# Kernel optimization log

Measured on AMD Instinct MI355X. Metric: run time of the kernel, lower is better.

The kernel has to match this reference:

```python
import jax, jax.numpy as jnp
import numpy as np

NLAT, NLON = 64, 64
CIN = 512
HEADS = 8


def _cc_weights(n):
    # Clenshaw-Curtis quadrature weights on [-1, 1] for nodes cos(k*pi/(n-1)),
    # as used by torch-harmonics for the 'equiangular' grid. Weights sum to 2.
    N = n - 1
    theta = np.pi * np.arange(n) / N
    m = N // 2
    j = np.arange(1, m + 1)
    b = np.where(2 * j == N, 1.0, 2.0)
    S = (b / (4.0 * j ** 2 - 1.0))[None, :] * np.cos(2.0 * j[None, :] * theta[:, None])
    w = 1.0 - S.sum(axis=1)
    c = np.full(n, 2.0)
    c[0] = 1.0
    c[-1] = 1.0
    return c * w / N


def _log_quad_weights(nlat, nlon):
    # _precompute_latitudes flips nodes/weights; then 2*pi*w/nlon tiled over lon.
    w = _cc_weights(nlat)[::-1].copy()
    qw = 2.0 * np.pi * w / nlon                       # (nlat,)
    qw = np.tile(qw[:, None], (1, nlon)).reshape(-1)  # (nlat*nlon,)
    return jnp.asarray(np.log(qw), dtype=jnp.float32)


def setup_inputs() -> dict:
    key = jax.random.key(0)
    ks = jax.random.split(key, 5)
    s_qkv = float(np.sqrt(3.0 / CIN))   # scale for q/k/v 1x1-conv weights
    s_proj = float(np.sqrt(3.0 / CIN))  # out_channels == CIN
    u = lambda k, sh, s: jax.random.uniform(k, sh, jnp.float32, -s, s)
    return dict(
        query=jax.random.normal(ks[0], (1, CIN, NLAT, NLON), jnp.float32),
        q_w=u(ks[1], (CIN, CIN), s_qkv), q_b=jnp.zeros((CIN,), jnp.float32),
        k_w=u(ks[2], (CIN, CIN), s_qkv), k_b=jnp.zeros((CIN,), jnp.float32),
        v_w=u(ks[3], (CIN, CIN), s_qkv), v_b=jnp.zeros((CIN,), jnp.float32),
        p_w=u(ks[4], (CIN, CIN), s_proj), p_b=jnp.zeros((CIN,), jnp.float32),
        log_quad_weights=_log_quad_weights(NLAT, NLON),
    )


def reference(query, q_w, q_b, k_w, k_b, v_w, v_b, p_w, p_b, log_quad_weights):
    B, C, H, W = query.shape
    hd = C // HEADS  # head dim (k_channels == out_channels == in_channels)

    def proj_tokens(x, w, b):
        # 1x1 conv == channel matmul, then split heads and flatten H*W tokens
        y = jnp.einsum('bihw,oi->bohw', x, w) + b[None, :, None, None]
        return y.reshape(B, HEADS, -1, H, W).transpose(0, 1, 3, 4, 2).reshape(B, HEADS, H * W, -1)

    q = proj_tokens(query, q_w, q_b)  # (B, heads, HW, hd)
    k = proj_tokens(query, k_w, k_b)  # self-attention: key/value default to query
    v = proj_tokens(query, v_w, v_b)

    scale = 1.0 / jnp.sqrt(jnp.asarray(hd, dtype=q.dtype))
    # additive log-quadrature bias over keys (broadcast over batch/head/query)
    logits = jnp.einsum('bhqd,bhkd->bhqk', q, k) * scale + log_quad_weights[None, None, None, :]
    attn = jax.nn.softmax(logits, axis=-1)
    out = jnp.einsum('bhqk,bhkd->bhqd', attn, v)          # (B, heads, HW, hd)
    out = out.transpose(0, 1, 3, 2).reshape(B, HEADS * hd, H, W)
    return jnp.einsum('bihw,oi->bohw', out, p_w) + p_b[None, :, None, None]
```

## Files before the change

kernel.cpp:

```cpp
#include <hip/hip_runtime.h>

typedef unsigned short u16;
typedef unsigned int u32;
typedef __bf16 bf16x8 __attribute__((ext_vector_type(8)));
typedef float f32x4 __attribute__((ext_vector_type(4)));
typedef unsigned short u16x4 __attribute__((ext_vector_type(4)));

#define LOG2E 1.4426950408889634f

#if __has_builtin(__builtin_amdgcn_exp2f)
#define EXP2F(x) __builtin_amdgcn_exp2f(x)
#else
#define EXP2F(x) exp2f(x)
#endif

__device__ __forceinline__ u16 f2bf(float f) {
    union { float f; u32 u; } a; a.f = f;
    u32 u = a.u;
    u += 0x7FFFu + ((u >> 16) & 1u);
    return (u16)(u >> 16);
}
__device__ __forceinline__ bf16x8 ldg8(const u16* p) {
    return *reinterpret_cast<const bf16x8*>(p);
}
#if __has_builtin(__builtin_amdgcn_cvt_pk_bf16_f32)
__device__ __forceinline__ u32 pack2(float a, float b) {
    auto r = __builtin_amdgcn_cvt_pk_bf16_f32(a, b);
    return __builtin_bit_cast(u32, r);
}
#else
__device__ __forceinline__ u32 pack2(float a, float b) {
    u32 ua = __float_as_uint(a) + 0x8000u;
    u32 ub = __float_as_uint(b) + 0x8000u;
    return __builtin_amdgcn_perm(ub, ua, 0x07060302);
}
#endif
__device__ __forceinline__ void async16(const void* g, void* l) {
    __builtin_amdgcn_global_load_lds(
        (const __attribute__((address_space(1))) u32*)g,
        (__attribute__((address_space(3))) u32*)l, 16, 0, 0);
}

#define MFMA16(a, b, c) __builtin_amdgcn_mfma_f32_16x16x32_bf16((a), (b), (c), 0, 0, 0)

__global__ __launch_bounds__(256) void prep(const float* __restrict__ X,
                                            u16* __restrict__ Xt,
                                            const float* __restrict__ s0,
                                            const float* __restrict__ s1,
                                            const float* __restrict__ s2,
                                            const float* __restrict__ s3,
                                            u16* __restrict__ Wqkv,
                                            u16* __restrict__ Wp,
                                            const float* __restrict__ lqw,
                                            float* __restrict__ lqw2g) {
    __shared__ u16 tile[64][65];
    const int tid = threadIdx.x;
    const int y = blockIdx.y;

    if (y < 8) {
        const int t0 = blockIdx.x * 64;
        const int c0 = y * 64;
#pragma unroll
        for (int i = 0; i < 16; ++i) {
            int idx = tid + i * 256;
            int r = idx >> 6, cc = idx & 63;
            tile[r][cc] = f2bf(X[(size_t)(c0 + r) * 4096 + t0 + cc]);
        }
        __syncthreads();
#pragma unroll
        for (int i = 0; i < 16; ++i) {
            int idx = tid + i * 256;
            int tr = idx >> 6, cc = idx & 63;
            Xt[(size_t)(t0 + tr) * 512 + c0 + cc] = tile[cc][tr];
        }
    } else if (y < 12) {
        const int m = y - 8;
        const float* s = (m == 0) ? s0 : (m == 1) ? s1 : (m == 2) ? s2 : s3;
        u16* d = (m == 3) ? Wp : Wqkv + (size_t)m * 262144;
#pragma unroll
        for (int j = 0; j < 4; ++j) {
            int i = blockIdx.x * 1024 + j * 256 + tid;
            float4 v = reinterpret_cast<const float4*>(s)[i];
            u16x4 o;
            o[0] = f2bf(v.x); o[1] = f2bf(v.y); o[2] = f2bf(v.z); o[3] = f2bf(v.w);
            reinterpret_cast<u16x4*>(d)[i] = o;
        }
    } else {
        if (blockIdx.x < 4) {
            int i = blockIdx.x * 256 + tid;
            float4 v = reinterpret_cast<const float4*>(lqw)[i];
            v.x *= LOG2E; v.y *= LOG2E; v.z *= LOG2E; v.w *= LOG2E;
            reinterpret_cast<float4*>(lqw2g)[i] = v;
        }
    }
}

__global__ __launch_bounds__(512, 2) void qkv_gemm(const u16* __restrict__ Wqkv,
                                                   const u16* __restrict__ Xt,
                                                   const float* __restrict__ qb,
                                                   const float* __restrict__ kb,
                                                   const float* __restrict__ vb,
                                                   u16* __restrict__ Qt,
                                                   u16* __restrict__ Kt,
                                                   u16* __restrict__ Vp) {
    __shared__ __align__(16) u16 Al[2][128 * 32];
    __shared__ __align__(16) u16 Bl[2][128 * 32];

    const int tid = threadIdx.x;
    const int w = tid >> 6, lane = tid & 63;
    const int quad = lane >> 4, lm = lane & 15;
    const int wm = w & 1, wn = w >> 1;
    const int n0 = blockIdx.x * 128;
    const int my = blockIdx.y;
    const int m0 = my * 128;

    const int arow = lane >> 2;
    const int sch = (lane & 3) ^ ((lane >> 3) & 3);
    const u16* agp = Wqkv + (size_t)(m0 + w * 16 + arow) * 512 + sch * 8;
    const u16* bgp = Xt + (size_t)(n0 + w * 16 + arow) * 512 + sch * 8;

    async16(agp, &Al[0][w * 16 * 32]);
    async16(bgp, &Bl[0][w * 16 * 32]);
    agp += 32; bgp += 32;

    const int FOFF = lm * 64 + ((quad ^ ((lm >> 1) & 3)) << 4);

    f32x4 acc[4][2];
#pragma unroll
    for (int mt = 0; mt < 4; ++mt)
#pragma unroll
        for (int bt = 0; bt < 2; ++bt) acc[mt][bt] = (f32x4){0.f, 0.f, 0.f, 0.f};

    __syncthreads();

    for (int s = 0; s < 16; ++s) {
        const int buf = s & 1;
        if (s < 15) {
            async16(agp, &Al[buf ^ 1][w * 16 * 32]);
            async16(bgp, &Bl[buf ^ 1][w * 16 * 32]);
            agp += 32; bgp += 32;
        }
        const char* Ab = (const char*)&Al[buf][0];
        const char* Bb = (const char*)&Bl[buf][0];
        bf16x8 af[4], bfr[2];
#pragma unroll
        for (int mt = 0; mt < 4; ++mt)
            af[mt] = *(const bf16x8*)(Ab + wm * 4096 + mt * 1024 + FOFF);
#pragma unroll
        for (int bt = 0; bt < 2; ++bt)
            bfr[bt] = *(const bf16x8*)(Bb + wn * 2048 + bt * 1024 + FOFF);
#pragma unroll
        for (int mt = 0; mt < 4; ++mt)
#pragma unroll
            for (int bt = 0; bt < 2; ++bt)
                acc[mt][bt] = MFMA16(af[mt], bfr[bt], acc[mt][bt]);
        __syncthreads();
    }

    const int mat = my >> 2;
    const float* bias = (mat == 0) ? qb : (mat == 1) ? kb : vb;
    const int chbase = (my & 3) * 128 + wm * 64 + quad * 4;

    if (mat < 2) {
        u16* out = mat ? Kt : Qt;
        const float sc = mat ? 1.0f : 0.125f * LOG2E;
#pragma unroll
        for (int mt = 0; mt < 4; ++mt) {
            const int ch = chbase + mt * 16;
            float4 bv = *(const float4*)(bias + ch);
            float bvf[4] = {bv.x, bv.y, bv.z, bv.w};
#pragma unroll
            for (int bt = 0; bt < 2; ++bt) {
                int tok = n0 + wn * 32 + bt * 16 + lm;
                u16x4 pk;
#pragma unroll
                for (int r = 0; r < 4; ++r)
                    pk[r] = f2bf((acc[mt][bt][r] + bvf[r]) * sc);
                *(u16x4*)(out + (size_t)tok * 512 + ch) = pk;
            }
        }
    } else {
#pragma unroll
        for (int mt = 0; mt < 4; ++mt) {
            const int ch = chbase + mt * 16;
            float4 bv = *(const float4*)(bias + ch);
            float bvf[4] = {bv.x, bv.y, bv.z, bv.w};
#pragma unroll
            for (int bt = 0; bt < 2; ++bt) {
                int g = bt * 16 + lm;
                int col = n0 + wn * 32 + 8 * ((g >> 2) & 3) + 4 * ((g >> 4) & 1) + (g & 3);
#pragma unroll
                for (int r = 0; r < 4; ++r)
                    Vp[(size_t)(ch + r) * 4096 + col] = f2bf(acc[mt][bt][r] + bvf[r]);
            }
        }
    }
}

__global__ __launch_bounds__(256, 2) void out_gemm(const u16* __restrict__ Wp,
                                                   const u16* __restrict__ Ot,
                                                   const float* __restrict__ pb,
                                                   float* __restrict__ out) {
    __shared__ __align__(16) u16 Al[2][128 * 32];
    __shared__ __align__(16) u16 Bl[2][64 * 32];

    const int tid = threadIdx.x;
    const int w = tid >> 6, lane = tid & 63;
    const int quad = lane >> 4, lm = lane & 15;
    const int wm = w & 1, wn = w >> 1;
    const int n0 = blockIdx.x * 64;
    const int m0 = blockIdx.y * 128;

    const int arow = lane >> 2;
    const int sch = (lane & 3) ^ ((lane >> 3) & 3);
    const u16* agp0 = Wp + (size_t)(m0 + w * 16 + arow) * 512 + sch * 8;
    const u16* agp1 = agp0 + (size_t)64 * 512;
    const u16* bgp = Ot + (size_t)(n0 + w * 16 + arow) * 512 + sch * 8;

    async16(agp0, &Al[0][w * 16 * 32]);
    async16(agp1, &Al[0][(64 + w * 16) * 32]);
    async16(bgp, &Bl[0][w * 16 * 32]);
    agp0 += 32; agp1 += 32; bgp += 32;

    const int FOFF = lm * 64 + ((quad ^ ((lm >> 1) & 3)) << 4);

    f32x4 acc[4][2];
#pragma unroll
    for (int mt = 0; mt < 4; ++mt)
#pragma unroll
        for (int bt = 0; bt < 2; ++bt) acc[mt][bt] = (f32x4){0.f, 0.f, 0.f, 0.f};

    __syncthreads();

    for (int s = 0; s < 16; ++s) {
        const int buf = s & 1;
        if (s < 15) {
            async16(agp0, &Al[buf ^ 1][w * 16 * 32]);
            async16(agp1, &Al[buf ^ 1][(64 + w * 16) * 32]);
            async16(bgp, &Bl[buf ^ 1][w * 16 * 32]);
            agp0 += 32; agp1 += 32; bgp += 32;
        }
        const char* Ab = (const char*)&Al[buf][0];
        const char* Bb = (const char*)&Bl[buf][0];
        bf16x8 af[4], bfr[2];
#pragma unroll
        for (int mt = 0; mt < 4; ++mt)
            af[mt] = *(const bf16x8*)(Ab + wm * 4096 + mt * 1024 + FOFF);
#pragma unroll
        for (int bt = 0; bt < 2; ++bt)
            bfr[bt] = *(const bf16x8*)(Bb + wn * 2048 + bt * 1024 + FOFF);
#pragma unroll
        for (int mt = 0; mt < 4; ++mt)
#pragma unroll
            for (int bt = 0; bt < 2; ++bt)
                acc[mt][bt] = MFMA16(af[mt], bfr[bt], acc[mt][bt]);
        __syncthreads();
    }

#pragma unroll
    for (int mt = 0; mt < 4; ++mt) {
        const int ch = m0 + wm * 64 + mt * 16 + quad * 4;
        float4 bv = *(const float4*)(pb + ch);
        float bvf[4] = {bv.x, bv.y, bv.z, bv.w};
#pragma unroll
        for (int bt = 0; bt < 2; ++bt) {
            int tok = n0 + wn * 32 + bt * 16 + lm;
#pragma unroll
            for (int r = 0; r < 4; ++r)
                out[(size_t)(ch + r) * 4096 + tok] = acc[mt][bt][r] + bvf[r];
        }
    }
}

__global__ __launch_bounds__(512, 4) void flash_attn(const u16* __restrict__ Qt,
                                                     const u16* __restrict__ Kt,
                                                     const u16* __restrict__ Vp,
                                                     const float* __restrict__ lqw2g,
                                                     u16* __restrict__ Ot) {
    __shared__ __align__(16) u16 kv[4][2][2][2048];

    const int tid = threadIdx.x;
    const int w = tid >> 6, lane = tid & 63;
    const int quad = lane >> 4, lm = lane & 15;
    const int qg = w & 1, quarter = w >> 1;
    const int h = blockIdx.y, hq = h * 64;
    const int q0 = blockIdx.x * 64 + qg * 32;
    const int kstart = quarter * 1024;

    char* kvb = (char*)&kv[0][0][0][0] + quarter * 16384;

    const int srow = lane >> 3;
    const int schunk = (lane & 7) ^ srow;
    const u16* kgp = Kt + (size_t)(kstart + qg * 16 + srow) * 512 + hq + schunk * 8;
    const u16* kgp8 = kgp + (size_t)8 * 512;
    const int dloc0 = qg * 32 + 2 * srow + (schunk >> 2);
    const u16* vgpA = Vp + (size_t)(hq + dloc0) * 4096 + kstart + (schunk & 3) * 8;
    const u16* vgpB = vgpA + (size_t)16 * 4096;

    {
        char* nb = kvb;
        async16(kgp, nb + qg * 2048);
        async16(kgp8, nb + qg * 2048 + 1024);
        async16(vgpA, nb + 4096 + qg * 2048);
        async16(vgpB, nb + 4096 + qg * 2048 + 1024);
        kgp += 32 * 512; kgp8 += 32 * 512; vgpA += 32; vgpB += 32;
    }

    const int A0 = lm * 128 + ((quad ^ (lm & 7)) << 4);
    const int A1 = A0 ^ 64;
    const int AV = (lm >> 1) * 128 +
                   ((((4 * (lm & 1) + quad)) ^ ((lm >> 1) & 7)) << 4);

    const u16* qbase = Qt + (size_t)(q0 + lm) * 512 + hq + quad * 8;
    const bf16x8 bq0a = ldg8(qbase);
    const bf16x8 bq1a = ldg8(qbase + 32);
    const bf16x8 bq0b = ldg8(qbase + 16 * 512);
    const bf16x8 bq1b = ldg8(qbase + 16 * 512 + 32);

    union { u32 u[4]; bf16x8 v; } onesu;
    onesu.u[0] = onesu.u[1] = onesu.u[2] = onesu.u[3] = 0x3F803F80u;
    const bf16x8 onesv = onesu.v;

    f32x4 acc_o[4][2];
#pragma unroll
    for (int mt = 0; mt < 4; ++mt) {
        acc_o[mt][0] = (f32x4){0.f, 0.f, 0.f, 0.f};
        acc_o[mt][1] = (f32x4){0.f, 0.f, 0.f, 0.f};
    }
    f32x4 acc_l[2];
    acc_l[0] = (f32x4){0.f, 0.f, 0.f, 0.f};
    acc_l[1] = (f32x4){0.f, 0.f, 0.f, 0.f};

    __syncthreads();

#define ATTN_STEP(BUF, KT0, DO_STAGE)                                          \
    {                                                                          \
        if (DO_STAGE) {                                                        \
            char* nb = kvb + (((BUF) ^ 1) * 8192);                             \
            async16(kgp, nb + qg * 2048);                                      \
            async16(kgp8, nb + qg * 2048 + 1024);                              \
            async16(vgpA, nb + 4096 + qg * 2048);                              \
            async16(vgpB, nb + 4096 + qg * 2048 + 1024);                       \
            kgp += 32 * 512; kgp8 += 32 * 512; vgpA += 32; vgpB += 32;         \
        }                                                                      \
        const char* Kb = kvb + (BUF) * 8192;                                   \
        const char* Vb = Kb + 4096;                                            \
        u32 pk[2][2][2];                                                       \
        _Pragma("unroll")                                                      \
        for (int nt = 0; nt < 2; ++nt) {                                       \
            bf16x8 k0 = *(const bf16x8*)(Kb + nt * 2048 + A0);                 \
            bf16x8 k1 = *(const bf16x8*)(Kb + nt * 2048 + A1);                 \
            f32x4 bias = *(const f32x4*)(lqw2g + (KT0) + nt * 16 + quad * 4);  \
            f32x4 a0 = MFMA16(k0, bq0a, bias);                                 \
            a0 = MFMA16(k1, bq1a, a0);                                         \
            f32x4 a1 = MFMA16(k0, bq0b, bias);                                 \
            a1 = MFMA16(k1, bq1b, a1);                                         \
            pk[nt][0][0] = pack2(EXP2F(a0[0]), EXP2F(a0[1]));                  \
            pk[nt][0][1] = pack2(EXP2F(a0[2]), EXP2F(a0[3]));                  \
            pk[nt][1][0] = pack2(EXP2F(a1[0]), EXP2F(a1[1]));                  \
            pk[nt][1][1] = pack2(EXP2F(a1[2]), EXP2F(a1[3]));                  \
        }                                                                      \
        union { u32 u[4]; bf16x8 v; } bb0, bb1;                                \
        bb0.u[0] = pk[0][0][0]; bb0.u[1] = pk[0][0][1];                        \
        bb0.u[2] = pk[1][0][0]; bb0.u[3] = pk[1][0][1];                        \
        bb1.u[0] = pk[0][1][0]; bb1.u[1] = pk[0][1][1];                        \
        bb1.u[2] = pk[1][1][0]; bb1.u[3] = pk[1][1][1];                        \
        _Pragma("unroll")                                                      \
        for (int mt = 0; mt < 4; ++mt) {                                       \
            bf16x8 vv = *(const bf16x8*)(Vb + mt * 1024 + AV);                 \
            acc_o[mt][0] = MFMA16(vv, bb0.v, acc_o[mt][0]);                    \
            acc_o[mt][1] = MFMA16(vv, bb1.v, acc_o[mt][1]);                    \
        }                                                                      \
        acc_l[0] = MFMA16(onesv, bb0.v, acc_l[0]);                             \
        acc_l[1] = MFMA16(onesv, bb1.v, acc_l[1]);                             \
        __syncthreads();                                                       \
    }

    for (int kt0 = kstart; kt0 < kstart + 1024; kt0 += 64) {
        ATTN_STEP(0, kt0, true)
        ATTN_STEP(1, kt0 + 32, (kt0 + 64 < kstart + 1024))
    }
#undef ATTN_STEP

    float* mbuf = (float*)&kv[0][0][0][0];
    if (quarter != 0) {
        const int widx = (quarter - 1) * 2 + qg;
        float* ob = mbuf + widx * 2048;
#pragma unroll
        for (int s = 0; s < 2; ++s)
#pragma unroll
            for (int mt = 0; mt < 4; ++mt)
                *(f32x4*)(ob + (s * 16 + lm) * 64 + mt * 16 + quad * 4) = acc_o[mt][s];
        if (quad == 0) {
            mbuf[12288 + widx * 32 + lm] = acc_l[0][0];
            mbuf[12288 + widx * 32 + 16 + lm] = acc_l[1][0];
        }
    }
    __syncthreads();
    if (quarter != 0) return;

#pragma unroll
    for (int s = 0; s < 2; ++s) {
        float lsum = acc_l[s][0];
#pragma unroll
        for (int p = 0; p < 3; ++p)
            lsum += mbuf[12288 + (p * 2 + qg) * 32 + s * 16 + lm];
        const float inv = 1.0f / lsum;
#pragma unroll
        for (int mt = 0; mt < 4; ++mt) {
            f32x4 o = acc_o[mt][s];
#pragma unroll
            for (int p = 0; p < 3; ++p)
                o += *(const f32x4*)(mbuf + (p * 2 + qg) * 2048 +
                                     (s * 16 + lm) * 64 + mt * 16 + quad * 4);
            u16x4 pkv;
#pragma unroll
            for (int r = 0; r < 4; ++r)
                pkv[r] = f2bf(o[r] * inv);
            *reinterpret_cast<u16x4*>(Ot + (size_t)(q0 + s * 16 + lm) * 512 +
                                      hq + mt * 16 + quad * 4) = pkv;
        }
    }
}

extern "C" void kernel_launch(void* const* d_in, const int* in_sizes, int n_in,
                              void* d_out, int out_size, void* d_ws, size_t ws_size,
                              hipStream_t stream) {
    (void)in_sizes; (void)n_in; (void)out_size; (void)ws_size;
    const float* X   = (const float*)d_in[0];
    const float* qw  = (const float*)d_in[1];
    const float* qb  = (const float*)d_in[2];
    const float* kw  = (const float*)d_in[3];
    const float* kb  = (const float*)d_in[4];
    const float* vw  = (const float*)d_in[5];
    const float* vb  = (const float*)d_in[6];
    const float* pw  = (const float*)d_in[7];
    const float* pb  = (const float*)d_in[8];
    const float* lqw = (const float*)d_in[9];

    const size_t E = (size_t)4096 * 512;
    const size_t WE = (size_t)512 * 512;
    u16* Xt    = (u16*)d_ws;
    u16* Qt    = Xt + E;
    u16* Kt    = Qt + E;
    u16* Vp    = Kt + E;
    u16* Wqkv  = Vp + E;
    u16* Wp    = Wqkv + 3 * WE;
    float* lqw2g = (float*)(Wp + WE);
    u16* Ot    = Xt;

    prep<<<dim3(64, 13), dim3(256), 0, stream>>>(X, Xt, qw, kw, vw, pw,
                                                 Wqkv, Wp, lqw, lqw2g);
    qkv_gemm<<<dim3(32, 12), dim3(512), 0, stream>>>(Wqkv, Xt, qb, kb, vb, Qt, Kt, Vp);
    flash_attn<<<dim3(64, 8), dim3(512), 0, stream>>>(Qt, Kt, Vp, lqw2g, Ot);
    out_gemm<<<dim3(64, 4), dim3(256), 0, stream>>>(Wp, Ot, pb, (float*)d_out);
}
```

Measured before the change: 86.85 us.

## Load K/V fragments directly from global memory instead of staging through LDS

Removes the double-buffered async LDS staging of K and V tiles and their per-step block barriers. Each wave now reads its K and V MFMA fragments straight from global memory (through cache), and LDS is used only for the final cross-quarter reduction, which gains an XOR swizzle to avoid bank conflicts. This drops barrier and LDS traffic and may raise occupancy through the smaller shared footprint. The cost is redundant global/L2 loads, since both query-group waves fetch the same K/V, and load latency is exposed unless the unroll-by-2 hides it.

```diff
diff --git a/kernel.cpp b/kernel.cpp
--- a/kernel.cpp
+++ b/kernel.cpp
@@ -277,7 +277,7 @@
                                                      const u16* __restrict__ Vp,
                                                      const float* __restrict__ lqw2g,
                                                      u16* __restrict__ Ot) {
-    __shared__ __align__(16) u16 kv[4][2][2][2048];
+    __shared__ __align__(16) float mbuf[6 * 2048 + 192];
 
     const int tid = threadIdx.x;
     const int w = tid >> 6, lane = tid & 63;
@@ -287,36 +287,15 @@
     const int q0 = blockIdx.x * 64 + qg * 32;
     const int kstart = quarter * 1024;
 
-    char* kvb = (char*)&kv[0][0][0][0] + quarter * 16384;
-
-    const int srow = lane >> 3;
-    const int schunk = (lane & 7) ^ srow;
-    const u16* kgp = Kt + (size_t)(kstart + qg * 16 + srow) * 512 + hq + schunk * 8;
-    const u16* kgp8 = kgp + (size_t)8 * 512;
-    const int dloc0 = qg * 32 + 2 * srow + (schunk >> 2);
-    const u16* vgpA = Vp + (size_t)(hq + dloc0) * 4096 + kstart + (schunk & 3) * 8;
-    const u16* vgpB = vgpA + (size_t)16 * 4096;
-
-    {
-        char* nb = kvb;
-        async16(kgp, nb + qg * 2048);
-        async16(kgp8, nb + qg * 2048 + 1024);
-        async16(vgpA, nb + 4096 + qg * 2048);
-        async16(vgpB, nb + 4096 + qg * 2048 + 1024);
-        kgp += 32 * 512; kgp8 += 32 * 512; vgpA += 32; vgpB += 32;
-    }
-
-    const int A0 = lm * 128 + ((quad ^ (lm & 7)) << 4);
-    const int A1 = A0 ^ 64;
-    const int AV = (lm >> 1) * 128 +
-                   ((((4 * (lm & 1) + quad)) ^ ((lm >> 1) & 7)) << 4);
-
     const u16* qbase = Qt + (size_t)(q0 + lm) * 512 + hq + quad * 8;
     const bf16x8 bq0a = ldg8(qbase);
     const bf16x8 bq1a = ldg8(qbase + 32);
     const bf16x8 bq0b = ldg8(qbase + 16 * 512);
     const bf16x8 bq1b = ldg8(qbase + 16 * 512 + 32);
 
+    const u16* kfp = Kt + (size_t)(kstart + lm) * 512 + hq + quad * 8;
+    const u16* vfp = Vp + (size_t)(hq + lm) * 4096 + kstart + quad * 8;
+
     union { u32 u[4]; bf16x8 v; } onesu;
     onesu.u[0] = onesu.u[1] = onesu.u[2] = onesu.u[3] = 0x3F803F80u;
     const bf16x8 onesv = onesu.v;
@@ -331,66 +310,52 @@
     acc_l[0] = (f32x4){0.f, 0.f, 0.f, 0.f};
     acc_l[1] = (f32x4){0.f, 0.f, 0.f, 0.f};
 
-    __syncthreads();
-
-#define ATTN_STEP(BUF, KT0, DO_STAGE)                                          \
-    {                                                                          \
-        if (DO_STAGE) {                                                        \
-            char* nb = kvb + (((BUF) ^ 1) * 8192);                             \
-            async16(kgp, nb + qg * 2048);                                      \
-            async16(kgp8, nb + qg * 2048 + 1024);                              \
-            async16(vgpA, nb + 4096 + qg * 2048);                              \
-            async16(vgpB, nb + 4096 + qg * 2048 + 1024);                       \
-            kgp += 32 * 512; kgp8 += 32 * 512; vgpA += 32; vgpB += 32;         \
-        }                                                                      \
-        const char* Kb = kvb + (BUF) * 8192;                                   \
-        const char* Vb = Kb + 4096;                                            \
-        u32 pk[2][2][2];                                                       \
-        _Pragma("unroll")                                                      \
-        for (int nt = 0; nt < 2; ++nt) {                                       \
-            bf16x8 k0 = *(const bf16x8*)(Kb + nt * 2048 + A0);                 \
-            bf16x8 k1 = *(const bf16x8*)(Kb + nt * 2048 + A1);                 \
-            f32x4 bias = *(const f32x4*)(lqw2g + (KT0) + nt * 16 + quad * 4);  \
-            f32x4 a0 = MFMA16(k0, bq0a, bias);                                 \
-            a0 = MFMA16(k1, bq1a, a0);                                         \
-            f32x4 a1 = MFMA16(k0, bq0b, bias);                                 \
-            a1 = MFMA16(k1, bq1b, a1);                                         \
-            pk[nt][0][0] = pack2(EXP2F(a0[0]), EXP2F(a0[1]));                  \
-            pk[nt][0][1] = pack2(EXP2F(a0[2]), EXP2F(a0[3]));                  \
-            pk[nt][1][0] = pack2(EXP2F(a1[0]), EXP2F(a1[1]));                  \
-            pk[nt][1][1] = pack2(EXP2F(a1[2]), EXP2F(a1[3]));                  \
-        }                                                                      \
-        union { u32 u[4]; bf16x8 v; } bb0, bb1;                                \
-        bb0.u[0] = pk[0][0][0]; bb0.u[1] = pk[0][0][1];                        \
-        bb0.u[2] = pk[1][0][0]; bb0.u[3] = pk[1][0][1];                        \
-        bb1.u[0] = pk[0][1][0]; bb1.u[1] = pk[0][1][1];                        \
-        bb1.u[2] = pk[1][1][0]; bb1.u[3] = pk[1][1][1];                        \
-        _Pragma("unroll")                                                      \
-        for (int mt = 0; mt < 4; ++mt) {                                       \
-            bf16x8 vv = *(const bf16x8*)(Vb + mt * 1024 + AV);                 \
-            acc_o[mt][0] = MFMA16(vv, bb0.v, acc_o[mt][0]);                    \
-            acc_o[mt][1] = MFMA16(vv, bb1.v, acc_o[mt][1]);                    \
-        }                                                                      \
-        acc_l[0] = MFMA16(onesv, bb0.v, acc_l[0]);                             \
-        acc_l[1] = MFMA16(onesv, bb1.v, acc_l[1]);                             \
-        __syncthreads();                                                       \
-    }
-
-    for (int kt0 = kstart; kt0 < kstart + 1024; kt0 += 64) {
-        ATTN_STEP(0, kt0, true)
-        ATTN_STEP(1, kt0 + 32, (kt0 + 64 < kstart + 1024))
-    }
-#undef ATTN_STEP
-
-    float* mbuf = (float*)&kv[0][0][0][0];
+#pragma unroll 2
+    for (int t = 0; t < 32; ++t) {
+        const int kt0 = kstart + t * 32;
+        u32 pk[2][2][2];
+#pragma unroll
+        for (int nt = 0; nt < 2; ++nt) {
+            const u16* kp = kfp + (size_t)(t * 32 + nt * 16) * 512;
+            bf16x8 k0 = ldg8(kp);
+            bf16x8 k1 = ldg8(kp + 32);
+            f32x4 bias = *(const f32x4*)(lqw2g + kt0 + nt * 16 + quad * 4);
+            f32x4 a0 = MFMA16(k0, bq0a, bias);
+            a0 = MFMA16(k1, bq1a, a0);
+            f32x4 a1 = MFMA16(k0, bq0b, bias);
+            a1 = MFMA16(k1, bq1b, a1);
+            pk[nt][0][0] = pack2(EXP2F(a0[0]), EXP2F(a0[1]));
+            pk[nt][0][1] = pack2(EXP2F(a0[2]), EXP2F(a0[3]));
+            pk[nt][1][0] = pack2(EXP2F(a1[0]), EXP2F(a1[1]));
+            pk[nt][1][1] = pack2(EXP2F(a1[2]), EXP2F(a1[3]));
+        }
+        union { u32 u[4]; bf16x8 v; } bb0, bb1;
+        bb0.u[0] = pk[0][0][0]; bb0.u[1] = pk[0][0][1];
+        bb0.u[2] = pk[1][0][0]; bb0.u[3] = pk[1][0][1];
+        bb1.u[0] = pk[0][1][0]; bb1.u[1] = pk[0][1][1];
+        bb1.u[2] = pk[1][1][0]; bb1.u[3] = pk[1][1][1];
+#pragma unroll
+        for (int mt = 0; mt < 4; ++mt) {
+            bf16x8 vv = ldg8(vfp + (size_t)(mt * 16) * 4096 + t * 32);
+            acc_o[mt][0] = MFMA16(vv, bb0.v, acc_o[mt][0]);
+            acc_o[mt][1] = MFMA16(vv, bb1.v, acc_o[mt][1]);
+        }
+        acc_l[0] = MFMA16(onesv, bb0.v, acc_l[0]);
+        acc_l[1] = MFMA16(onesv, bb1.v, acc_l[1]);
+    }
+
     if (quarter != 0) {
         const int widx = (quarter - 1) * 2 + qg;
         float* ob = mbuf + widx * 2048;
 #pragma unroll
-        for (int s = 0; s < 2; ++s)
-#pragma unroll
-            for (int mt = 0; mt < 4; ++mt)
-                *(f32x4*)(ob + (s * 16 + lm) * 64 + mt * 16 + quad * 4) = acc_o[mt][s];
+        for (int s = 0; s < 2; ++s) {
+            const int r = s * 16 + lm;
+#pragma unroll
+            for (int mt = 0; mt < 4; ++mt) {
+                const int sl = (mt * 4 + quad) ^ (r & 15);
+                *(f32x4*)(ob + r * 64 + sl * 4) = acc_o[mt][s];
+            }
+        }
         if (quad == 0) {
             mbuf[12288 + widx * 32 + lm] = acc_l[0][0];
             mbuf[12288 + widx * 32 + 16 + lm] = acc_l[1][0];
@@ -401,6 +366,7 @@
 
 #pragma unroll
     for (int s = 0; s < 2; ++s) {
+        const int r = s * 16 + lm;
         float lsum = acc_l[s][0];
 #pragma unroll
         for (int p = 0; p < 3; ++p)
@@ -408,15 +374,15 @@
         const float inv = 1.0f / lsum;
 #pragma unroll
         for (int mt = 0; mt < 4; ++mt) {
+            const int sl = (mt * 4 + quad) ^ (r & 15);
             f32x4 o = acc_o[mt][s];
 #pragma unroll
             for (int p = 0; p < 3; ++p)
-                o += *(const f32x4*)(mbuf + (p * 2 + qg) * 2048 +
-                                     (s * 16 + lm) * 64 + mt * 16 + quad * 4);
+                o += *(const f32x4*)(mbuf + (p * 2 + qg) * 2048 + r * 64 + sl * 4);
             u16x4 pkv;
 #pragma unroll
-            for (int r = 0; r < 4; ++r)
-                pkv[r] = f2bf(o[r] * inv);
+            for (int r2 = 0; r2 < 4; ++r2)
+                pkv[r2] = f2bf(o[r2] * inv);
             *reinterpret_cast<u16x4*>(Ot + (size_t)(q0 + s * 16 + lm) * 512 +
                                       hq + mt * 16 + quad * 4) = pkv;
         }
```

Result: slower. 158.7 us (+82.8%).
